# Kernel optimization log

Measured on AMD Instinct MI355X. Metric: run time of the kernel, lower is better.

The kernel has to match this reference:

```python
import jax, jax.numpy as jnp
import numpy as np

DIM = 4096
N_HEADS = 32
HEAD_DIM = 128
N_KV_HEADS = 8
KV_REPEATS = N_HEADS // N_KV_HEADS
SLIDING_WINDOW = 4096
SEQLEN = 2048
ROPE_THETA = 10000.0


def calculate_rope(x, cos_freq, sin_freq):
    # x: (S, H, D); cos/sin: (S, D//2). Rotates interleaved pairs (Mistral RoPE).
    S, H, D = x.shape
    xr = x.reshape(S, H, D // 2, 2)
    x1, x2 = xr[..., 0], xr[..., 1]
    c = cos_freq[:, None, :]
    s = sin_freq[:, None, :]
    o1 = x1 * c - x2 * s
    o2 = x1 * s + x2 * c
    return jnp.stack([o1, o2], axis=-1).reshape(S, H, D)


def setup_inputs() -> dict:
    key = jax.random.key(0)
    k0, k1, k2 = jax.random.split(key, 3)
    x = jax.random.normal(k0, (SEQLEN, DIM), dtype=jnp.float32)
    positions = jnp.arange(SEQLEN, dtype=jnp.int32)
    # RoPE frequencies
    inv_freq = 1.0 / (ROPE_THETA ** (np.arange(0, HEAD_DIM, 2, dtype=np.float32) / HEAD_DIM))
    angles = np.arange(SEQLEN, dtype=np.float32)[:, None] * inv_freq[None, :]
    cos_freq = jnp.asarray(np.cos(angles), dtype=jnp.float32)
    sin_freq = jnp.asarray(np.sin(angles), dtype=jnp.float32)
    # additive causal + sliding-window mask: 0 where allowed, -1e9 where masked
    i = np.arange(SEQLEN)
    allowed = (i[None, :] <= i[:, None]) & ((i[:, None] - i[None, :]) < SLIDING_WINDOW)
    mask = jnp.asarray(np.where(allowed, 0.0, -1e9), dtype=jnp.float32)
    cache_k = jnp.zeros((SLIDING_WINDOW, N_KV_HEADS, HEAD_DIM), dtype=jnp.float32)
    cache_v = jnp.zeros((SLIDING_WINDOW, N_KV_HEADS, HEAD_DIM), dtype=jnp.float32)
    total_head_dim = (N_HEADS + 2 * N_KV_HEADS) * HEAD_DIM
    Wqkv = jax.random.normal(k1, (total_head_dim, DIM), dtype=jnp.float32) * 0.02
    Wo = jax.random.normal(k2, (DIM, N_HEADS * HEAD_DIM), dtype=jnp.float32) * 0.02
    return {"x": x, "cos_freq": cos_freq, "sin_freq": sin_freq, "positions": positions,
            "mask": mask, "cache_k": cache_k, "cache_v": cache_v, "Wqkv": Wqkv, "Wo": Wo}


def reference(x, cos_freq, sin_freq, positions, mask, cache_k, cache_v, Wqkv, Wo):
    # Prefill branch (positions.shape[0] > 1) of Attention.__call__
    seqlen = x.shape[0]
    scale = HEAD_DIM ** (-0.5)
    s1 = N_HEADS * HEAD_DIM
    s2 = s1 + N_KV_HEADS * HEAD_DIM
    xqkv = x @ Wqkv.T                                  # (S, 6144)
    xq, xk, xv = jnp.split(xqkv, [s1, s2], axis=-1)
    xq = xq.reshape(seqlen, N_HEADS, HEAD_DIM)
    xk = xk.reshape(seqlen, N_KV_HEADS, HEAD_DIM)
    xv = xv.reshape(seqlen, N_KV_HEADS, HEAD_DIM)
    xq = calculate_rope(xq, cos_freq, sin_freq)
    xk = calculate_rope(xk, cos_freq, sin_freq)
    # KV-cache update (scatter; positions all in range here)
    cache_k = cache_k.at[positions, :, :].set(xk[positions, :, :], mode="drop")
    cache_v = cache_v.at[positions, :, :].set(xv[positions, :, :], mode="drop")
    # GQA repeat: (S, n_kv, D) -> (S, n_heads, D)
    k = jnp.repeat(xk, KV_REPEATS, axis=1)
    v = jnp.repeat(xv, KV_REPEATS, axis=1)
    q = jnp.transpose(xq, (1, 0, 2))                   # (H, S, D)
    k = jnp.transpose(k, (1, 0, 2))
    v = jnp.transpose(v, (1, 0, 2))
    scores = jnp.einsum("hqd,hkd->hqk", q, k) * scale  # (H, S, S)
    scores = scores + mask[jnp.newaxis, ...]
    probs = jax.nn.softmax(scores.astype(jnp.float32), axis=-1).astype(q.dtype)
    out = jnp.einsum("hqk,hkd->hqd", probs, v)         # (H, S, D)
    out = jnp.transpose(out, (1, 0, 2)).reshape(seqlen, -1)
    output = out @ Wo.T                                # (S, dim)
    return (output, cache_k, cache_v)
```

## Files before the change

kernel.cpp:

```cpp
#include <hip/hip_runtime.h>
#include <stdint.h>

typedef __bf16   bf16x8 __attribute__((ext_vector_type(8)));
typedef float    f32x4  __attribute__((ext_vector_type(4)));
typedef uint16_t u16x8  __attribute__((ext_vector_type(8)));

__device__ __forceinline__ uint16_t f2bf(float f) {
  uint32_t b = __builtin_bit_cast(uint32_t, f);
  b += 0x7fffu + ((b >> 16) & 1u);
  return (uint16_t)(b >> 16);
}
__device__ __forceinline__ float bf2f(uint16_t u) {
  return __builtin_bit_cast(float, ((uint32_t)u) << 16);
}
__device__ __forceinline__ u16x8 ldcvt8(const float* __restrict__ p) {
  f32x4 lo = *(const f32x4*)p;
  f32x4 hi = *(const f32x4*)(p + 4);
  u16x8 o;
  o[0] = f2bf(lo[0]); o[1] = f2bf(lo[1]); o[2] = f2bf(lo[2]); o[3] = f2bf(lo[3]);
  o[4] = f2bf(hi[0]); o[5] = f2bf(hi[1]); o[6] = f2bf(hi[2]); o[7] = f2bf(hi[3]);
  return o;
}

typedef const __attribute__((address_space(1))) uint32_t cga_u32;
typedef __attribute__((address_space(3))) uint32_t lds_u32;
__device__ __forceinline__ void gload16(const uint16_t* g, uint16_t* l) {
  __builtin_amdgcn_global_load_lds((cga_u32*)g, (lds_u32*)l, 16, 0, 0);
}

__global__ __launch_bounds__(256) void cast_kernel(const float* __restrict__ in,
                                                   uint16_t* __restrict__ out, int n8) {
  int i = blockIdx.x * 256 + threadIdx.x;
  if (i >= n8) return;
  u16x8 o = ldcvt8(in + (size_t)i * 8);
  *(u16x8*)(out + (size_t)i * 8) = o;
}

__global__ __launch_bounds__(256) void copy2_kernel(const float* __restrict__ a, float* __restrict__ da,
                                                    const float* __restrict__ b, float* __restrict__ db,
                                                    int n4) {
  int i = blockIdx.x * 256 + threadIdx.x;
  if (i >= n4) return;
  *(f32x4*)(da + (size_t)i * 4) = *(const f32x4*)(a + (size_t)i * 4);
  *(f32x4*)(db + (size_t)i * 4) = *(const f32x4*)(b + (size_t)i * 4);
}

template <int OUT_BF16>
__global__ __launch_bounds__(256) void gemm_nt_bf16(const uint16_t* __restrict__ A,
                                                    const uint16_t* __restrict__ B,
                                                    void* __restrict__ Cout,
                                                    int M, int N, int K) {
  __shared__ __align__(16) uint16_t As[128 * 32];
  __shared__ __align__(16) uint16_t Bs[128 * 32];
  const int tid = threadIdx.x;
  const int lane = tid & 63, wave = tid >> 6;
  const int l16 = lane & 15, quad = lane >> 4;
  const int wm = (wave & 1) << 6, wn = (wave >> 1) << 6;
  const int bm = blockIdx.y, bn = blockIdx.x;

  f32x4 acc[4][4] = {};

  const int srow = wave * 16 + (lane >> 2);
  const int schunk = lane & 3;
  const uint16_t* Ag = A + (size_t)(bm * 128 + srow) * K + schunk * 8;
  const uint16_t* Bg = B + (size_t)(bn * 128 + srow) * K + schunk * 8;
  const size_t rs64 = (size_t)64 * K;
  uint16_t* AsD0 = &As[srow * 32 + schunk * 8];
  uint16_t* AsD1 = AsD0 + 64 * 32;
  uint16_t* BsD0 = &Bs[srow * 32 + schunk * 8];
  uint16_t* BsD1 = BsD0 + 64 * 32;

  for (int k0 = 0; k0 < K; k0 += 32) {
    gload16(Ag, AsD0);
    gload16(Ag + rs64, AsD1);
    gload16(Bg, BsD0);
    gload16(Bg + rs64, BsD1);
    Ag += 32; Bg += 32;
    __syncthreads();
    bf16x8 af[4], bfr[4];
#pragma unroll
    for (int i = 0; i < 4; i++) {
      af[i]  = __builtin_bit_cast(bf16x8, *(const u16x8*)&As[(wm + i * 16 + l16) * 32 + quad * 8]);
      bfr[i] = __builtin_bit_cast(bf16x8, *(const u16x8*)&Bs[(wn + i * 16 + l16) * 32 + quad * 8]);
    }
#pragma unroll
    for (int i = 0; i < 4; i++)
#pragma unroll
      for (int j = 0; j < 4; j++)
        acc[i][j] = __builtin_amdgcn_mfma_f32_16x16x32_bf16(af[i], bfr[j], acc[i][j], 0, 0, 0);
    __syncthreads();
  }

  const int row0 = bm * 128 + wm + quad * 4;
  const int col0 = bn * 128 + wn + l16;
#pragma unroll
  for (int i = 0; i < 4; i++)
#pragma unroll
    for (int j = 0; j < 4; j++)
#pragma unroll
      for (int r = 0; r < 4; r++) {
        size_t idx = (size_t)(row0 + i * 16 + r) * N + (col0 + j * 16);
        if constexpr (OUT_BF16) ((uint16_t*)Cout)[idx] = f2bf(acc[i][j][r]);
        else                    ((float*)Cout)[idx]    = acc[i][j][r];
      }
}

template <int A_BF16, int OUT_BF16>
__global__ __launch_bounds__(256) void gemm_bt(const void* __restrict__ Ap,
                                               const float* __restrict__ B,
                                               void* __restrict__ Cout, int M, int N, int K) {
  constexpr int PAD = 40;
  __shared__ __align__(16) uint16_t As[128 * PAD];
  __shared__ __align__(16) uint16_t Bs[128 * PAD];
  const int tid = threadIdx.x;
  const int lane = tid & 63, wave = tid >> 6;
  const int l16 = lane & 15, quad = lane >> 4;
  const int wm = (wave & 1) << 6, wn = (wave >> 1) << 6;
  const int bm = blockIdx.y, bn = blockIdx.x;

  f32x4 acc[4][4] = {};

  const int srow = tid >> 2;
  const int scol = (tid & 3) << 3;
  const size_t aoff = (size_t)(bm * 128 + srow) * K + scol;
  const uint16_t* Agh = (const uint16_t*)Ap + aoff;
  const float*    Agf = (const float*)Ap + aoff;
  const float*    Bg  = B + (size_t)(bn * 128 + srow) * K + scol;
  const size_t rstride = (size_t)64 * K;

  for (int k0 = 0; k0 < K; k0 += 32) {
    u16x8 a0, a1;
    if constexpr (A_BF16) {
      a0 = *(const u16x8*)Agh;
      a1 = *(const u16x8*)(Agh + rstride);
      Agh += 32;
    } else {
      a0 = ldcvt8(Agf);
      a1 = ldcvt8(Agf + rstride);
      Agf += 32;
    }
    u16x8 b0 = ldcvt8(Bg);
    u16x8 b1 = ldcvt8(Bg + rstride);
    Bg += 32;
    __syncthreads();
    *(u16x8*)&As[srow * PAD + scol] = a0;
    *(u16x8*)&As[(srow + 64) * PAD + scol] = a1;
    *(u16x8*)&Bs[srow * PAD + scol] = b0;
    *(u16x8*)&Bs[(srow + 64) * PAD + scol] = b1;
    __syncthreads();
    bf16x8 af[4], bfr[4];
#pragma unroll
    for (int i = 0; i < 4; i++) {
      af[i]  = __builtin_bit_cast(bf16x8, *(const u16x8*)&As[(wm + i * 16 + l16) * PAD + quad * 8]);
      bfr[i] = __builtin_bit_cast(bf16x8, *(const u16x8*)&Bs[(wn + i * 16 + l16) * PAD + quad * 8]);
    }
#pragma unroll
    for (int i = 0; i < 4; i++)
#pragma unroll
      for (int j = 0; j < 4; j++)
        acc[i][j] = __builtin_amdgcn_mfma_f32_16x16x32_bf16(af[i], bfr[j], acc[i][j], 0, 0, 0);
  }

  const int row0 = bm * 128 + wm + quad * 4;
  const int col0 = bn * 128 + wn + l16;
#pragma unroll
  for (int i = 0; i < 4; i++)
#pragma unroll
    for (int j = 0; j < 4; j++)
#pragma unroll
      for (int r = 0; r < 4; r++) {
        size_t idx = (size_t)(row0 + i * 16 + r) * N + (col0 + j * 16);
        if constexpr (OUT_BF16) ((uint16_t*)Cout)[idx] = f2bf(acc[i][j][r]);
        else                    ((float*)Cout)[idx]    = acc[i][j][r];
      }
}

__global__ __launch_bounds__(256) void rope_kernel(const uint16_t* __restrict__ xqkv,
    const float* __restrict__ cosf, const float* __restrict__ sinf,
    const int* __restrict__ pos,
    uint16_t* __restrict__ qb, uint16_t* __restrict__ kb, uint16_t* __restrict__ vb,
    float* __restrict__ ck, float* __restrict__ cv) {
  const float QS = 0.12751743f;
  const int s = blockIdx.x;
  const int e0 = (blockIdx.y * 256 + threadIdx.x) * 8;
  const int head = e0 >> 7;
  const int d0 = e0 & 127;
  u16x8 u = *(const u16x8*)(xqkv + (size_t)s * 6144 + e0);
  float x[8];
#pragma unroll
  for (int j = 0; j < 8; j++) x[j] = bf2f(u[j]);

  if (head < 40) {
    const int i0 = d0 >> 1;
    f32x4 c4 = *(const f32x4*)(cosf + (size_t)s * 64 + i0);
    f32x4 s4 = *(const f32x4*)(sinf + (size_t)s * 64 + i0);
    float o[8];
#pragma unroll
    for (int kk = 0; kk < 4; kk++) {
      float x1 = x[2 * kk], x2 = x[2 * kk + 1];
      o[2 * kk]     = x1 * c4[kk] - x2 * s4[kk];
      o[2 * kk + 1] = x1 * s4[kk] + x2 * c4[kk];
    }
    if (head < 32) {
      u16x8 ob;
#pragma unroll
      for (int j = 0; j < 8; j++) ob[j] = f2bf(o[j] * QS);
      *(u16x8*)(qb + (size_t)s * 4096 + head * 128 + d0) = ob;
    } else {
      u16x8 ob;
#pragma unroll
      for (int j = 0; j < 8; j++) ob[j] = f2bf(o[j]);
      int kvh = head - 32;
      *(u16x8*)(kb + ((size_t)kvh * 2048 + s) * 128 + d0) = ob;
      int p = pos[s];
      if ((unsigned)p < 4096u) {
        float* dst = ck + ((size_t)p * 8 + kvh) * 128 + d0;
#pragma unroll
        for (int j = 0; j < 8; j++) dst[j] = o[j];
      }
    }
  } else {
    int kvh = head - 40;
    *(u16x8*)(vb + ((size_t)kvh * 2048 + s) * 128 + d0) = u;
    int p = pos[s];
    if ((unsigned)p < 4096u) {
      float* dst = cv + ((size_t)p * 8 + kvh) * 128 + d0;
#pragma unroll
      for (int j = 0; j < 8; j++) dst[j] = x[j];
    }
  }
}

__global__ __launch_bounds__(256) void vtrans_kernel(const uint16_t* __restrict__ vb,
                                                     uint16_t* __restrict__ vt) {
  __shared__ __align__(16) uint16_t t[32 * 72];
  const int h = blockIdx.z;
  const int s0 = blockIdx.x * 64, d0 = blockIdx.y * 32;
  const uint16_t* in = vb + (size_t)h * 2048 * 128;
  uint16_t* out = vt + (size_t)h * 128 * 2048;
  const int tid = threadIdx.x;
  {
    int r = tid >> 2, c8 = (tid & 3) * 8;
    u16x8 v = *(const u16x8*)(in + (size_t)(s0 + r) * 128 + d0 + c8);
#pragma unroll
    for (int j = 0; j < 8; j++) t[(c8 + j) * 72 + r] = v[j];
  }
  __syncthreads();
  {
    int r = tid >> 3, c8 = (tid & 7) * 8;
    u16x8 v = *(const u16x8*)&t[r * 72 + c8];
    *(u16x8*)(out + (size_t)(d0 + r) * 2048 + s0 + c8) = v;
  }
}

__global__ __launch_bounds__(256) void flash_kernel(const uint16_t* __restrict__ Qb,
    const uint16_t* __restrict__ Kb, const uint16_t* __restrict__ Vtb,
    uint16_t* __restrict__ Ob) {
  __shared__ __align__(16) uint16_t Ks[64 * 128];
  __shared__ __align__(16) uint16_t Vts[128 * 64];
  __shared__ __align__(16) uint16_t Ps[4][16 * 64];
  const int tid = threadIdx.x;
  const int lane = tid & 63, wave = tid >> 6;
  const int l16 = lane & 15, quad = lane >> 4;
  const int h = blockIdx.y, kvh = h >> 2;
  const uint16_t* Kg = Kb + (size_t)kvh * 2048 * 128;
  const uint16_t* Vg = Vtb + (size_t)kvh * 128 * 2048;

  u16x8 kreg[4], vreg[4];
  const int krr = tid >> 4, kcb = (tid & 15) * 16;
  const int vrr = tid >> 3, vcb = (tid & 7) * 16;

  for (int ph = 0; ph < 2; ph++) {
    const int qtile = ph ? (int)blockIdx.x : 31 - (int)blockIdx.x;
    const int qb = qtile * 64;
    const int nch = qtile + 1;
    const int qmax = qb + wave * 16 + 15;

    bf16x8 qf[4];
    {
      const uint16_t* Qg = Qb + (size_t)(qb + wave * 16 + l16) * 4096 + h * 128 + quad * 8;
#pragma unroll
      for (int dc = 0; dc < 4; dc++)
        qf[dc] = __builtin_bit_cast(bf16x8, *(const u16x8*)(Qg + dc * 32));
    }

    f32x4 oacc[8] = {};
    float m_run[4], l_run[4];
#pragma unroll
    for (int r = 0; r < 4; r++) { m_run[r] = -1e30f; l_run[r] = 0.f; }

#pragma unroll
    for (int i = 0; i < 4; i++)
      kreg[i] = *(const u16x8*)(Kg + (size_t)(krr + i * 16) * 128 + kcb / 2);
#pragma unroll
    for (int i = 0; i < 4; i++)
      vreg[i] = *(const u16x8*)(Vg + (size_t)(vrr + i * 32) * 2048 + vcb / 2);

    for (int ch = 0; ch < nch; ch++) {
      const int cb = ch * 64;
#pragma unroll
      for (int i = 0; i < 4; i++) {
        int r = krr + i * 16;
        *(u16x8*)((char*)Ks + r * 256 + (kcb ^ ((r & 7) << 4))) = kreg[i];
      }
#pragma unroll
      for (int i = 0; i < 4; i++) {
        int r = vrr + i * 32;
        *(u16x8*)((char*)Vts + r * 128 + (vcb ^ ((r & 7) << 4))) = vreg[i];
      }
      __syncthreads();

      if (ch + 1 < nch) {
        const int nb = cb + 64;
#pragma unroll
        for (int i = 0; i < 4; i++)
          kreg[i] = *(const u16x8*)(Kg + (size_t)(nb + krr + i * 16) * 128 + kcb / 2);
#pragma unroll
        for (int i = 0; i < 4; i++)
          vreg[i] = *(const u16x8*)(Vg + (size_t)(vrr + i * 32) * 2048 + nb + vcb / 2);
      }

      f32x4 sacc[4] = {};
      __builtin_amdgcn_s_setprio(1);
#pragma unroll
      for (int ni = 0; ni < 4; ni++) {
        if (cb + ni * 16 <= qmax) {
#pragma unroll
          for (int dc = 0; dc < 4; dc++) {
            int r = ni * 16 + l16;
            bf16x8 kf = __builtin_bit_cast(bf16x8,
                *(const u16x8*)((const char*)Ks + r * 256 + ((dc * 64 + quad * 16) ^ ((r & 7) << 4))));
            sacc[ni] = __builtin_amdgcn_mfma_f32_16x16x32_bf16(qf[dc], kf, sacc[ni], 0, 0, 0);
          }
        }
      }
      __builtin_amdgcn_s_setprio(0);

      float p[4][4], alpha[4];
#pragma unroll
      for (int reg = 0; reg < 4; reg++) {
        const int q = qb + wave * 16 + quad * 4 + reg;
        float mx = -1e30f;
#pragma unroll
        for (int ni = 0; ni < 4; ni++) {
          float sv = sacc[ni][reg];
          if (cb + ni * 16 + l16 > q) sv = -1e30f;
          p[ni][reg] = sv;
          mx = fmaxf(mx, sv);
        }
#pragma unroll
        for (int off = 8; off >= 1; off >>= 1)
          mx = fmaxf(mx, __shfl_xor(mx, off, 64));
        float mn = fmaxf(m_run[reg], mx);
        alpha[reg] = __builtin_amdgcn_exp2f(m_run[reg] - mn);
        m_run[reg] = mn;
        float rs = 0.f;
#pragma unroll
        for (int ni = 0; ni < 4; ni++) {
          float e = __builtin_amdgcn_exp2f(p[ni][reg] - mn);
          p[ni][reg] = e;
          rs += e;
        }
#pragma unroll
        for (int off = 8; off >= 1; off >>= 1)
          rs += __shfl_xor(rs, off, 64);
        l_run[reg] = l_run[reg] * alpha[reg] + rs;
      }

#pragma unroll
      for (int dt = 0; dt < 8; dt++)
#pragma unroll
        for (int reg = 0; reg < 4; reg++)
          oacc[dt][reg] *= alpha[reg];

      uint16_t* Pw = Ps[wave];
#pragma unroll
      for (int ni = 0; ni < 4; ni++)
#pragma unroll
        for (int reg = 0; reg < 4; reg++) {
          int r = quad * 4 + reg;
          *(uint16_t*)((char*)Pw + r * 128 + ((ni * 32 + l16 * 2) ^ ((r & 7) << 4))) =
              f2bf(p[ni][reg]);
        }

      __builtin_amdgcn_s_setprio(1);
#pragma unroll
      for (int kc = 0; kc < 2; kc++) {
        if (cb + kc * 32 <= qmax) {
          bf16x8 pf = __builtin_bit_cast(bf16x8,
              *(const u16x8*)((const char*)Pw + l16 * 128 + ((kc * 64 + quad * 16) ^ ((l16 & 7) << 4))));
#pragma unroll
          for (int dt = 0; dt < 8; dt++) {
            int r = dt * 16 + l16;
            bf16x8 vf = __builtin_bit_cast(bf16x8,
                *(const u16x8*)((const char*)Vts + r * 128 + ((kc * 64 + quad * 16) ^ ((r & 7) << 4))));
            oacc[dt] = __builtin_amdgcn_mfma_f32_16x16x32_bf16(pf, vf, oacc[dt], 0, 0, 0);
          }
        }
      }
      __builtin_amdgcn_s_setprio(0);

      __syncthreads();
    }

#pragma unroll
    for (int dt = 0; dt < 8; dt++)
#pragma unroll
      for (int reg = 0; reg < 4; reg++) {
        float o = oacc[dt][reg] / l_run[reg];
        int row = qb + wave * 16 + quad * 4 + reg;
        int col = h * 128 + dt * 16 + l16;
        Ob[(size_t)row * 4096 + col] = f2bf(o);
      }
  }
}

extern "C" void kernel_launch(void* const* d_in, const int* in_sizes, int n_in,
                              void* d_out, int out_size, void* d_ws, size_t ws_size,
                              hipStream_t stream) {
  const float* x     = (const float*)d_in[0];
  const float* cosf  = (const float*)d_in[1];
  const float* sinf  = (const float*)d_in[2];
  const int*   pos   = (const int*)d_in[3];
  const float* ck_in = (const float*)d_in[5];
  const float* cv_in = (const float*)d_in[6];
  const float* Wqkv  = (const float*)d_in[7];
  const float* Wo    = (const float*)d_in[8];

  float* out    = (float*)d_out;
  float* ck_out = out + (size_t)2048 * 4096;
  float* cv_out = ck_out + (size_t)4096 * 8 * 128;

  char* ws = (char*)d_ws;

  if (ws_size >= 104857600ull) {
    uint16_t* xqkv_bf = (uint16_t*)(ws);
    uint16_t* attn_bf = (uint16_t*)(ws);
    uint16_t* x_bf    = (uint16_t*)(ws + 25165824);
    uint16_t* q_bf    = (uint16_t*)(ws + 25165824);
    uint16_t* k_bf    = (uint16_t*)(ws + 41943040);
    uint16_t* v_bf    = (uint16_t*)(ws + 46137344);
    uint16_t* vt_bf   = (uint16_t*)(ws + 50331648);
    uint16_t* wq_bf   = (uint16_t*)(ws + 54525952);
    uint16_t* wo_bf   = (uint16_t*)(ws + 54525952);

    cast_kernel<<<4096, 256, 0, stream>>>(x, x_bf, 1048576);
    cast_kernel<<<12288, 256, 0, stream>>>(Wqkv, wq_bf, 3145728);

    gemm_nt_bf16<1><<<dim3(48, 16), 256, 0, stream>>>(x_bf, wq_bf, xqkv_bf, 2048, 6144, 4096);

    copy2_kernel<<<4096, 256, 0, stream>>>(ck_in, ck_out, cv_in, cv_out, 1048576);

    rope_kernel<<<dim3(2048, 3), 256, 0, stream>>>(xqkv_bf, cosf, sinf, pos,
                                                   q_bf, k_bf, v_bf, ck_out, cv_out);

    vtrans_kernel<<<dim3(32, 4, 8), 256, 0, stream>>>(v_bf, vt_bf);

    flash_kernel<<<dim3(16, 32), 256, 0, stream>>>(q_bf, k_bf, vt_bf, attn_bf);

    cast_kernel<<<8192, 256, 0, stream>>>(Wo, wo_bf, 2097152);

    gemm_nt_bf16<0><<<dim3(32, 16), 256, 0, stream>>>(attn_bf, wo_bf, out, 2048, 4096, 4096);
  } else {
    uint16_t* xqkv_bf = (uint16_t*)(ws);
    uint16_t* attn_bf = (uint16_t*)(ws);
    uint16_t* q_bf    = (uint16_t*)(ws + 25165824);
    uint16_t* k_bf    = (uint16_t*)(ws + 41943040);
    uint16_t* v_bf    = (uint16_t*)(ws + 46137344);
    uint16_t* vt_bf   = (uint16_t*)(ws + 50331648);

    gemm_bt<0, 1><<<dim3(48, 16), 256, 0, stream>>>(x, Wqkv, xqkv_bf, 2048, 6144, 4096);
    copy2_kernel<<<4096, 256, 0, stream>>>(ck_in, ck_out, cv_in, cv_out, 1048576);
    rope_kernel<<<dim3(2048, 3), 256, 0, stream>>>(xqkv_bf, cosf, sinf, pos,
                                                   q_bf, k_bf, v_bf, ck_out, cv_out);
    vtrans_kernel<<<dim3(32, 4, 8), 256, 0, stream>>>(v_bf, vt_bf);
    flash_kernel<<<dim3(16, 32), 256, 0, stream>>>(q_bf, k_bf, vt_bf, attn_bf);
    gemm_bt<1, 0><<<dim3(32, 16), 256, 0, stream>>>(attn_bf, Wo, out, 2048, 4096, 4096);
  }
}
```

Baseline: 614.6 us.

## Add 256x256-tile bf16 GEMM with 8 waves and LDS multi-buffering for projections

Adds a new GEMM kernel with 256x256 output tiles, 512 threads and a 64-wide K step. It triple-buffers A and double-buffers B in LDS via direct global-to-LDS loads with swizzled offsets, and interleaves fragment loads with MFMA phases using barriers and setprio. Both the QKV and output projections switch to it, falling back to the old 128-tile kernel if the launch fails. The aim is more data reuse per tile and better overlap of loads with compute. The cost is fewer blocks (192 and 128), which may underfill the GPU's CUs, plus about 160KB of LDS per block.

```diff
diff --git a/kernel.cpp b/kernel.cpp
--- a/kernel.cpp
+++ b/kernel.cpp
@@ -43,6 +43,166 @@
   if (i >= n4) return;
   *(f32x4*)(da + (size_t)i * 4) = *(const f32x4*)(a + (size_t)i * 4);
   *(f32x4*)(db + (size_t)i * 4) = *(const f32x4*)(b + (size_t)i * 4);
+}
+
+template <int OUT_BF16>
+__global__ __launch_bounds__(512, 2) void gemm256(const uint16_t* __restrict__ A,
+                                                  const uint16_t* __restrict__ B,
+                                                  void* __restrict__ Cout,
+                                                  int M, int N, int K) {
+  __shared__ __align__(16) uint16_t AS[3][256 * 64];
+  __shared__ __align__(16) uint16_t BS[2][256 * 64];
+  const int tid = threadIdx.x;
+  const int lane = tid & 63, wave = tid >> 6;
+  const int l16 = lane & 15, quad = lane >> 4;
+  const int wm = wave >> 2;
+  const int wn = wave & 3;
+  const int bm = blockIdx.y, bn = blockIdx.x;
+  const int NT = K >> 6;
+
+  f32x4 acc[8][4] = {};
+
+  const int sr = tid >> 3;
+  const int sc = ((tid & 7) ^ (sr & 7)) << 3;
+  const uint16_t* Asrc = A + (size_t)(bm * 256 + sr) * K + sc;
+  const uint16_t* Bsrc = B + (size_t)(bn * 256 + sr) * K + sc;
+  const size_t rs64 = (size_t)64 * K;
+
+  int aoff[8][2], boff[4][2];
+#pragma unroll
+  for (int mr = 0; mr < 8; mr++)
+#pragma unroll
+    for (int ks = 0; ks < 2; ks++)
+      aoff[mr][ks] = (wm * 128 + mr * 16 + l16) * 128 +
+                     (((ks << 6) | (quad << 4)) ^ ((l16 & 7) << 4));
+#pragma unroll
+  for (int nr = 0; nr < 4; nr++)
+#pragma unroll
+    for (int ks = 0; ks < 2; ks++)
+      boff[nr][ks] = (wn * 64 + nr * 16 + l16) * 128 +
+                     (((ks << 6) | (quad << 4)) ^ ((l16 & 7) << 4));
+
+  auto stageA = [&](int buf, int h, int t) {
+    const uint16_t* s = Asrc + (size_t)(h * 128) * K + (size_t)t * 64;
+    uint16_t* d = &AS[buf][h * 8192 + tid * 8];
+    gload16(s, d);
+    gload16(s + rs64, d + 4096);
+  };
+  auto stageB = [&](int buf, int h, int t) {
+    const uint16_t* s = Bsrc + (size_t)(h * 128) * K + (size_t)t * 64;
+    uint16_t* d = &BS[buf][h * 8192 + tid * 8];
+    gload16(s, d);
+    gload16(s + rs64, d + 4096);
+  };
+
+  stageA(0, 0, 0); stageA(0, 1, 0); stageB(0, 0, 0); stageB(0, 1, 0);
+  stageA(1, 0, 1); stageA(1, 1, 1);
+  asm volatile("s_waitcnt vmcnt(4)" ::: "memory");
+  __builtin_amdgcn_s_barrier();
+
+  int ca = 0;
+  for (int t = 0; t < NT; t++) {
+    const int cb = t & 1, nb = cb ^ 1;
+    const int na3 = (ca + 2 >= 3) ? ca - 1 : ca + 2;
+    const char* Ab = (const char*)AS[ca];
+    const char* Bb = (const char*)BS[cb];
+    bf16x8 aF[4][2], bF[4][2];
+
+#pragma unroll
+    for (int m4 = 0; m4 < 4; m4++)
+#pragma unroll
+      for (int ks = 0; ks < 2; ks++)
+        aF[m4][ks] = __builtin_bit_cast(bf16x8, *(const u16x8*)(Ab + aoff[m4][ks]));
+#pragma unroll
+    for (int n2 = 0; n2 < 2; n2++)
+#pragma unroll
+      for (int ks = 0; ks < 2; ks++)
+        bF[n2][ks] = __builtin_bit_cast(bf16x8, *(const u16x8*)(Bb + boff[n2][ks]));
+    if (t + 1 < NT) stageB(nb, 0, t + 1);
+    __builtin_amdgcn_s_barrier();
+    asm volatile("s_waitcnt lgkmcnt(0)" ::: "memory");
+    __builtin_amdgcn_sched_barrier(0);
+    __builtin_amdgcn_s_setprio(1);
+#pragma unroll
+    for (int m4 = 0; m4 < 4; m4++)
+#pragma unroll
+      for (int n2 = 0; n2 < 2; n2++)
+#pragma unroll
+        for (int ks = 0; ks < 2; ks++)
+          acc[m4][n2] = __builtin_amdgcn_mfma_f32_16x16x32_bf16(aF[m4][ks], bF[n2][ks], acc[m4][n2], 0, 0, 0);
+    __builtin_amdgcn_s_setprio(0);
+    __builtin_amdgcn_s_barrier();
+
+#pragma unroll
+    for (int n2 = 0; n2 < 2; n2++)
+#pragma unroll
+      for (int ks = 0; ks < 2; ks++)
+        bF[2 + n2][ks] = __builtin_bit_cast(bf16x8, *(const u16x8*)(Bb + boff[2 + n2][ks]));
+    if (t + 1 < NT) stageB(nb, 1, t + 1);
+    __builtin_amdgcn_s_barrier();
+    asm volatile("s_waitcnt lgkmcnt(0)" ::: "memory");
+    __builtin_amdgcn_sched_barrier(0);
+    __builtin_amdgcn_s_setprio(1);
+#pragma unroll
+    for (int m4 = 0; m4 < 4; m4++)
+#pragma unroll
+      for (int n2 = 0; n2 < 2; n2++)
+#pragma unroll
+        for (int ks = 0; ks < 2; ks++)
+          acc[m4][2 + n2] = __builtin_amdgcn_mfma_f32_16x16x32_bf16(aF[m4][ks], bF[2 + n2][ks], acc[m4][2 + n2], 0, 0, 0);
+    __builtin_amdgcn_s_setprio(0);
+    __builtin_amdgcn_s_barrier();
+
+#pragma unroll
+    for (int m4 = 0; m4 < 4; m4++)
+#pragma unroll
+      for (int ks = 0; ks < 2; ks++)
+        aF[m4][ks] = __builtin_bit_cast(bf16x8, *(const u16x8*)(Ab + aoff[4 + m4][ks]));
+    if (t + 2 < NT) stageA(na3, 0, t + 2);
+    __builtin_amdgcn_s_barrier();
+    asm volatile("s_waitcnt lgkmcnt(0)" ::: "memory");
+    __builtin_amdgcn_sched_barrier(0);
+    __builtin_amdgcn_s_setprio(1);
+#pragma unroll
+    for (int m4 = 0; m4 < 4; m4++)
+#pragma unroll
+      for (int n2 = 0; n2 < 2; n2++)
+#pragma unroll
+        for (int ks = 0; ks < 2; ks++)
+          acc[4 + m4][n2] = __builtin_amdgcn_mfma_f32_16x16x32_bf16(aF[m4][ks], bF[n2][ks], acc[4 + m4][n2], 0, 0, 0);
+    __builtin_amdgcn_s_setprio(0);
+    __builtin_amdgcn_s_barrier();
+
+    if (t + 2 < NT) stageA(na3, 1, t + 2);
+    if (t < NT - 2) asm volatile("s_waitcnt vmcnt(4)" ::: "memory");
+    else            asm volatile("s_waitcnt vmcnt(0)" ::: "memory");
+    __builtin_amdgcn_s_barrier();
+    __builtin_amdgcn_s_setprio(1);
+#pragma unroll
+    for (int m4 = 0; m4 < 4; m4++)
+#pragma unroll
+      for (int n2 = 0; n2 < 2; n2++)
+#pragma unroll
+        for (int ks = 0; ks < 2; ks++)
+          acc[4 + m4][2 + n2] = __builtin_amdgcn_mfma_f32_16x16x32_bf16(aF[m4][ks], bF[2 + n2][ks], acc[4 + m4][2 + n2], 0, 0, 0);
+    __builtin_amdgcn_s_setprio(0);
+    __builtin_amdgcn_s_barrier();
+
+    ca = (ca == 2) ? 0 : ca + 1;
+  }
+
+  const int row0 = bm * 256 + wm * 128 + quad * 4;
+  const int col0 = bn * 256 + wn * 64 + l16;
+#pragma unroll
+  for (int mr = 0; mr < 8; mr++)
+#pragma unroll
+    for (int nr = 0; nr < 4; nr++)
+#pragma unroll
+      for (int r = 0; r < 4; r++) {
+        size_t idx = (size_t)(row0 + mr * 16 + r) * N + (col0 + nr * 16);
+        if constexpr (OUT_BF16) ((uint16_t*)Cout)[idx] = f2bf(acc[mr][nr][r]);
+        else                    ((float*)Cout)[idx]    = acc[mr][nr][r];
+      }
 }
 
 template <int OUT_BF16>
@@ -447,7 +607,12 @@
     cast_kernel<<<4096, 256, 0, stream>>>(x, x_bf, 1048576);
     cast_kernel<<<12288, 256, 0, stream>>>(Wqkv, wq_bf, 3145728);
 
-    gemm_nt_bf16<1><<<dim3(48, 16), 256, 0, stream>>>(x_bf, wq_bf, xqkv_bf, 2048, 6144, 4096);
+    bool ok256 = true;
+    gemm256<1><<<dim3(24, 8), 512, 0, stream>>>(x_bf, wq_bf, xqkv_bf, 2048, 6144, 4096);
+    if (hipGetLastError() != hipSuccess) {
+      ok256 = false;
+      gemm_nt_bf16<1><<<dim3(48, 16), 256, 0, stream>>>(x_bf, wq_bf, xqkv_bf, 2048, 6144, 4096);
+    }
 
     copy2_kernel<<<4096, 256, 0, stream>>>(ck_in, ck_out, cv_in, cv_out, 1048576);
 
@@ -460,7 +625,13 @@
 
     cast_kernel<<<8192, 256, 0, stream>>>(Wo, wo_bf, 2097152);
 
-    gemm_nt_bf16<0><<<dim3(32, 16), 256, 0, stream>>>(attn_bf, wo_bf, out, 2048, 4096, 4096);
+    if (ok256) {
+      gemm256<0><<<dim3(16, 8), 512, 0, stream>>>(attn_bf, wo_bf, out, 2048, 4096, 4096);
+      if (hipGetLastError() != hipSuccess)
+        gemm_nt_bf16<0><<<dim3(32, 16), 256, 0, stream>>>(attn_bf, wo_bf, out, 2048, 4096, 4096);
+    } else {
+      gemm_nt_bf16<0><<<dim3(32, 16), 256, 0, stream>>>(attn_bf, wo_bf, out, 2048, 4096, 4096);
+    }
   } else {
     uint16_t* xqkv_bf = (uint16_t*)(ws);
     uint16_t* attn_bf = (uint16_t*)(ws);
```

After: 606.1 us. About the same (-1.4%).
